# Kernel tuning notes

Hardware: AMD Instinct MI355X
Metric: run time of the kernel (lower is better)

The kernel has to match this reference:

```python
import jax, jax.numpy as jnp
import numpy as np
from jax import lax

B = 256; D_IN = 2048; HID = 2048; NSEG = 10; D_CTX = 1024; OUT = 100; NI = 205
KW_PCT = 0.05
K = int(round(KW_PCT * HID))  # 102 winners per sample per layer
W_DENSITY = 0.05      # weight_sparsity = 0.95
DEND_DENSITY = 0.05   # dendrite_weight_sparsity = 0.95


def setup_inputs() -> dict:
    key = jax.random.key(0)
    ks = jax.random.split(key, 16)
    def u(k, shape, bound):
        return jax.random.uniform(k, shape, minval=-bound, maxval=bound, dtype=jnp.float32)
    inp = {}
    inp["x"] = jax.random.normal(ks[0], (B, D_IN), jnp.float32)
    inp["context"] = jax.random.normal(ks[1], (B, D_CTX), jnp.float32)
    # layer 1 FF weights: modified kaiming, input density 1.0 -> bound = 1/sqrt(fan_in)
    inp["W1"] = u(ks[2], (HID, D_IN), 1.0 / np.sqrt(D_IN))
    inp["b1"] = jnp.zeros((HID,), jnp.float32)
    # dendrites: input density 1.0 (context_percent_on=1), weight density 0.05
    dend_bound = 1.0 / np.sqrt(DEND_DENSITY * D_CTX)
    inp["segW1"] = u(ks[3], (HID, NSEG, D_CTX), dend_bound)
    inp["maskW1"] = (jax.random.uniform(ks[4], (HID, D_IN)) < W_DENSITY).astype(jnp.float32)
    inp["maskS1"] = (jax.random.uniform(ks[5], (HID, NSEG, D_CTX)) < DEND_DENSITY).astype(jnp.float32)
    # layer 2 FF weights: input density = kw_percent_on (k-winners upstream)
    inp["W2"] = u(ks[6], (HID, HID), 1.0 / np.sqrt(KW_PCT * HID))
    inp["b2"] = jnp.zeros((HID,), jnp.float32)
    inp["segW2"] = u(ks[7], (HID, NSEG, D_CTX), dend_bound)
    inp["maskW2"] = (jax.random.uniform(ks[8], (HID, HID)) < W_DENSITY).astype(jnp.float32)
    inp["maskS2"] = (jax.random.uniform(ks[9], (HID, NSEG, D_CTX)) < DEND_DENSITY).astype(jnp.float32)
    # Dale (EiDense) output head: non-negative excitatory/inhibitory factors
    s = 1.0 / np.sqrt(HID)
    inp["Wex_out"] = jax.random.uniform(ks[10], (OUT, HID), dtype=jnp.float32) * s
    inp["Wix_out"] = jax.random.uniform(ks[11], (1, HID), dtype=jnp.float32) * s
    inp["Wei_out"] = jax.random.uniform(ks[12], (OUT, 1), dtype=jnp.float32)
    inp["b_out"] = jnp.zeros((OUT,), jnp.float32)
    return inp


def _kwinners(y, k):
    # keep top-k activations per row, zero the rest (boost_strength=0)
    vals, idxs = lax.top_k(y, k)  # [B, k]
    rows = jnp.arange(y.shape[0])[:, None]
    return jnp.zeros_like(y).at[rows, idxs].set(vals)


def _dendritic_layer(x, context, W, b, segW, maskW, maskS):
    # sparse-masked feedforward projection
    y = x @ (W * maskW).T + b  # [B, HID]
    # per-unit dendrite segment activations from context
    d = jnp.einsum('bc,usc->bus', context, segW * maskS)  # [B, HID, NSEG]
    # absolute-max gating: pick segment with max |activation|, gate by sigmoid
    sel = jnp.argmax(jnp.abs(d), axis=-1)  # [B, HID]
    chosen = jnp.take_along_axis(d, sel[..., None], axis=-1)[..., 0]
    y = y * jax.nn.sigmoid(chosen)
    return _kwinners(y, K)


def reference(x, context, W1, b1, segW1, maskW1, maskS1, W2, b2, segW2, maskW2, maskS2, Wex_out, Wix_out, Wei_out, b_out):
    h = _dendritic_layer(x, context, W1, b1, segW1, maskW1, maskS1)
    h = _dendritic_layer(h, context, W2, b2, segW2, maskW2, maskS2)
    # EiDense output head: W = Wex - Wei @ Wix (Dale's law), no output nonlinearity
    W_out = Wex_out - Wei_out @ Wix_out  # [OUT, HID]
    return h @ W_out.T + b_out
```

## Files before the change

### kernel.cpp

```cpp
#include <hip/hip_runtime.h>
#include <math.h>

#define B_SZ   256
#define D_IN   2048
#define HID    2048
#define NSEG   10
#define D_CTX  1024
#define OUT_N  100
#define KWIN   102
#define CAP    256

typedef float f32x4 __attribute__((ext_vector_type(4)));

__device__ __forceinline__ f32x4 ntld4(const float* p) {
  return __builtin_nontemporal_load((const f32x4*)p);
}

__device__ __forceinline__ unsigned f2key(float f) {
  unsigned b = __float_as_uint(f);
  return (b & 0x80000000u) ? ~b : (b | 0x80000000u);
}
__device__ __forceinline__ float key2f(unsigned k) {
  return (k & 0x80000000u) ? __uint_as_float(k & 0x7FFFFFFFu) : __uint_as_float(~k);
}

__global__ __launch_bounds__(256) void transpose2_k(const float* __restrict__ xsrc,
                                                    float* __restrict__ xdst,
                                                    const float* __restrict__ csrc,
                                                    float* __restrict__ cdst) {
  __shared__ float tile[32][33];
  int bid = blockIdx.x;
  const float* src; float* dst; int cols;
  const int NX = (D_IN / 32) * (B_SZ / 32);
  if (bid < NX) { src = xsrc; dst = xdst; cols = D_IN; }
  else { bid -= NX; src = csrc; dst = cdst; cols = D_CTX; }
  int nbx = cols / 32;
  int bx = bid % nbx, by = bid / nbx;
  int c0 = bx * 32, r0 = by * 32;
  int tx = threadIdx.x & 31, ty = threadIdx.x >> 5;
  for (int i = ty; i < 32; i += 8)
    tile[i][tx] = src[(r0 + i) * cols + (c0 + tx)];
  __syncthreads();
  for (int i = ty; i < 32; i += 8)
    dst[(c0 + i) * B_SZ + (r0 + tx)] = tile[tx][i];
}

__device__ __forceinline__ int compact_wave(const float* __restrict__ wrow,
                                            const float* __restrict__ mrow,
                                            int len4, float2* pairs, int* scnt) {
  const int t = threadIdx.x & 63;
  if (t == 0) *scnt = 0;
  __builtin_amdgcn_wave_barrier();
  for (int e = t; e < len4; e += 64) {
    f32x4 w = ntld4(wrow + 4 * e);
    f32x4 m = ntld4(mrow + 4 * e);
    bool n0 = (m.x != 0.f), n1 = (m.y != 0.f), n2 = (m.z != 0.f), n3 = (m.w != 0.f);
    int nz = (int)n0 + (int)n1 + (int)n2 + (int)n3;
    if (nz) {
      int pos = atomicAdd(scnt, nz);
      int c = e << 2;
      if (n0) { if (pos < CAP) pairs[pos] = make_float2(w.x, __int_as_float(c));     pos++; }
      if (n1) { if (pos < CAP) pairs[pos] = make_float2(w.y, __int_as_float(c + 1)); pos++; }
      if (n2) { if (pos < CAP) pairs[pos] = make_float2(w.z, __int_as_float(c + 2)); pos++; }
      if (n3) { if (pos < CAP) pairs[pos] = make_float2(w.w, __int_as_float(c + 3)); pos++; }
    }
  }
  __builtin_amdgcn_wave_barrier();
  int c = *scnt;
  return c > CAP ? CAP : c;
}

__device__ __forceinline__ int store_seg(const f32x4 w[4], const f32x4 m[4],
                                         float2* pairs, int* scnt) {
  const int t = threadIdx.x & 63;
  if (t == 0) *scnt = 0;
  __builtin_amdgcn_wave_barrier();
#pragma unroll
  for (int i = 0; i < 4; ++i) {
    int e = t + 64 * i;
    f32x4 ww = w[i], mm = m[i];
    bool n0 = (mm.x != 0.f), n1 = (mm.y != 0.f), n2 = (mm.z != 0.f), n3 = (mm.w != 0.f);
    int nz = (int)n0 + (int)n1 + (int)n2 + (int)n3;
    if (nz) {
      int pos = atomicAdd(scnt, nz);
      int c = e << 2;
      if (n0) { if (pos < CAP) pairs[pos] = make_float2(ww.x, __int_as_float(c));     pos++; }
      if (n1) { if (pos < CAP) pairs[pos] = make_float2(ww.y, __int_as_float(c + 1)); pos++; }
      if (n2) { if (pos < CAP) pairs[pos] = make_float2(ww.z, __int_as_float(c + 2)); pos++; }
      if (n3) { if (pos < CAP) pairs[pos] = make_float2(ww.w, __int_as_float(c + 3)); pos++; }
    }
  }
  __builtin_amdgcn_wave_barrier();
  int c = *scnt;
  return c > CAP ? CAP : c;
}

__device__ __forceinline__ void load_seg(const float* __restrict__ wrow,
                                         const float* __restrict__ mrow,
                                         f32x4 w[4], f32x4 m[4]) {
  const int t = threadIdx.x & 63;
#pragma unroll
  for (int i = 0; i < 4; ++i) {
    w[i] = ntld4(wrow + 4 * (t + 64 * i));
    m[i] = ntld4(mrow + 4 * (t + 64 * i));
  }
}

__device__ __forceinline__ void gather_dot(const float* __restrict__ src,
                                           const float2* pairs, int cnt,
                                           int t4, float out4[4]) {
  float acc[4][4];
#pragma unroll
  for (int s = 0; s < 4; ++s)
#pragma unroll
    for (int i = 0; i < 4; ++i) acc[s][i] = 0.f;
  int j = 0;
  for (; j + 8 <= cnt; j += 8) {
#pragma unroll
    for (int s = 0; s < 8; ++s) {
      float2 p = pairs[j + s];
      const f32x4 cv = *(const f32x4*)(src + (__float_as_int(p.y) << 8) + t4);
      acc[s & 3][0] += cv.x * p.x; acc[s & 3][1] += cv.y * p.x;
      acc[s & 3][2] += cv.z * p.x; acc[s & 3][3] += cv.w * p.x;
    }
  }
  for (; j < cnt; ++j) {
    float2 p = pairs[j];
    const f32x4 cv = *(const f32x4*)(src + (__float_as_int(p.y) << 8) + t4);
    acc[0][0] += cv.x * p.x; acc[0][1] += cv.y * p.x;
    acc[0][2] += cv.z * p.x; acc[0][3] += cv.w * p.x;
  }
#pragma unroll
  for (int i = 0; i < 4; ++i)
    out4[i] = (acc[0][i] + acc[1][i]) + (acc[2][i] + acc[3][i]);
}

__global__ __launch_bounds__(256, 3) void dend_kernel(
    const float* __restrict__ W1, const float* __restrict__ maskW1, const float* __restrict__ b1,
    const float* __restrict__ segW1, const float* __restrict__ maskS1,
    const float* __restrict__ segW2, const float* __restrict__ maskS2,
    const float* __restrict__ xT, const float* __restrict__ ctxT,
    float* __restrict__ y1T, float* __restrict__ gate2T) {
  __shared__ float2 pairs_s[4][CAP];
  __shared__ int scnt_s[4];
  const int wave = threadIdx.x >> 6;
  const int t = threadIdx.x & 63, t4 = t * 4;
  float2* pairs = pairs_s[wave];
  int* scnt = &scnt_s[wave];
  const int row = blockIdx.x * 4 + wave;

  const bool isL1 = (row < HID);
  const int u = isL1 ? row : (row - HID);
  const float* segW = (isL1 ? segW1 : segW2) + (size_t)u * NSEG * D_CTX;
  const float* maskS = (isL1 ? maskS1 : maskS2) + (size_t)u * NSEG * D_CTX;

  float bestA[4] = {-1.f, -1.f, -1.f, -1.f};
  float chosen[4] = {0.f, 0.f, 0.f, 0.f};
  float ff[4] = {0.f, 0.f, 0.f, 0.f};

  f32x4 w[4], m[4];
  if (isL1) {
    int cnt = compact_wave(W1 + (size_t)u * D_IN, maskW1 + (size_t)u * D_IN,
                           D_IN / 4, pairs, scnt);
    load_seg(segW, maskS, w, m);
    gather_dot(xT, pairs, cnt, t4, ff);
  } else {
    load_seg(segW, maskS, w, m);
  }

  for (int s = 0; s < NSEG; ++s) {
    int cnt = store_seg(w, m, pairs, scnt);
    if (s + 1 < NSEG)
      load_seg(segW + (s + 1) * D_CTX, maskS + (s + 1) * D_CTX, w, m);
    float d[4];
    gather_dot(ctxT, pairs, cnt, t4, d);
#pragma unroll
    for (int i = 0; i < 4; ++i) {
      float a = fabsf(d[i]);
      if (a > bestA[i]) { bestA[i] = a; chosen[i] = d[i]; }
    }
  }

  if (isL1) {
    float bb = b1[u];
    float4 o;
    o.x = (ff[0] + bb) / (1.f + expf(-chosen[0]));
    o.y = (ff[1] + bb) / (1.f + expf(-chosen[1]));
    o.z = (ff[2] + bb) / (1.f + expf(-chosen[2]));
    o.w = (ff[3] + bb) / (1.f + expf(-chosen[3]));
    *(float4*)(y1T + (size_t)u * B_SZ + t4) = o;
  } else {
    float4 g;
    g.x = 1.f / (1.f + expf(-chosen[0]));
    g.y = 1.f / (1.f + expf(-chosen[1]));
    g.z = 1.f / (1.f + expf(-chosen[2]));
    g.w = 1.f / (1.f + expf(-chosen[3]));
    *(float4*)(gate2T + (size_t)u * B_SZ + t4) = g;
  }
}

__global__ __launch_bounds__(256, 4) void ff2_kernel(
    const float* __restrict__ W2, const float* __restrict__ maskW2, const float* __restrict__ b2,
    const float* __restrict__ h1T, const float* __restrict__ gate2T, float* __restrict__ y2T) {
  __shared__ float2 pairs_s[4][CAP];
  __shared__ int scnt_s[4];
  const int wave = threadIdx.x >> 6;
  const int t = threadIdx.x & 63, t4 = t * 4;
  const int u = blockIdx.x * 4 + wave;
  int cnt = compact_wave(W2 + (size_t)u * HID, maskW2 + (size_t)u * HID,
                         HID / 4, pairs_s[wave], &scnt_s[wave]);
  float acc[4];
  gather_dot(h1T, pairs_s[wave], cnt, t4, acc);
  float bb = b2[u];
  float4 g = *(const float4*)(gate2T + (size_t)u * B_SZ + t4);
  float4 o;
  o.x = (acc[0] + bb) * g.x; o.y = (acc[1] + bb) * g.y;
  o.z = (acc[2] + bb) * g.z; o.w = (acc[3] + bb) * g.w;
  *(float4*)(y2T + (size_t)u * B_SZ + t4) = o;
}

__global__ __launch_bounds__(256) void topk_kernel(const float* __restrict__ yT,
                                                   float* __restrict__ dst, int mode) {
  const int b = blockIdx.x, t = threadIdx.x;
  __shared__ int hist[256];
  __shared__ int sfx[256];
  __shared__ unsigned sPref;
  __shared__ int sRem;
  unsigned myk[8];
#pragma unroll
  for (int i = 0; i < 8; ++i)
    myk[i] = f2key(yT[(size_t)(t * 8 + i) * B_SZ + b]);
  unsigned pref = 0;
  int rem = KWIN;
  for (int shift = 24; shift >= 0; shift -= 8) {
    hist[t] = 0;
    __syncthreads();
    unsigned hiMask = (shift == 24) ? 0u : (0xFFFFFFFFu << (shift + 8));
#pragma unroll
    for (int i = 0; i < 8; ++i) {
      unsigned k = myk[i];
      if ((k & hiMask) == pref) atomicAdd(&hist[(k >> shift) & 255], 1);
    }
    __syncthreads();
    sfx[t] = hist[t];
    __syncthreads();
    for (int off = 1; off < 256; off <<= 1) {
      int add = (t + off < 256) ? sfx[t + off] : 0;
      __syncthreads();
      sfx[t] += add;
      __syncthreads();
    }
    int s_incl = sfx[t];
    int s_excl = (t == 255) ? 0 : sfx[t + 1];
    if (s_incl >= rem && s_excl < rem) {
      sPref = pref | (((unsigned)t) << shift);
      sRem = rem - s_excl;
    }
    __syncthreads();
    pref = sPref;
    rem = sRem;
    __syncthreads();
  }
  int eq = 0;
#pragma unroll
  for (int i = 0; i < 8; ++i) eq += (myk[i] == pref) ? 1 : 0;
  sfx[t] = eq;
  __syncthreads();
  for (int off = 1; off < 256; off <<= 1) {
    int add = (t >= off) ? sfx[t - off] : 0;
    __syncthreads();
    sfx[t] += add;
    __syncthreads();
  }
  int excl = sfx[t] - eq;
  int taken = 0;
#pragma unroll
  for (int i = 0; i < 8; ++i) {
    unsigned k = myk[i];
    bool keep;
    if (k > pref) keep = true;
    else if (k == pref) { keep = (excl + taken) < rem; taken++; }
    else keep = false;
    float f = keep ? key2f(k) : 0.f;
    int uu = t * 8 + i;
    if (mode == 0) dst[(size_t)uu * B_SZ + b] = f;
    else dst[(size_t)b * HID + uu] = f;
  }
}

__global__ __launch_bounds__(256) void out_kernel(
    const float* __restrict__ h2, const float* __restrict__ Wex, const float* __restrict__ Wix,
    const float* __restrict__ Wei, const float* __restrict__ bo, float* __restrict__ out) {
  const int b = blockIdx.x, t = threadIdx.x;
  __shared__ float hrow[HID];
  __shared__ float red[256];
  float part = 0.f;
#pragma unroll
  for (int i = 0; i < 8; ++i) {
    int u = t + 256 * i;
    float v = h2[(size_t)b * HID + u];
    hrow[u] = v;
    part += v * Wix[u];
  }
  red[t] = part;
  __syncthreads();
  for (int off = 128; off > 0; off >>= 1) {
    if (t < off) red[t] += red[t + off];
    __syncthreads();
  }
  float S = red[0];
  const int w = t >> 6, l = t & 63;
  for (int o = w; o < OUT_N; o += 4) {
    float acc = 0.f;
    const float* wr = Wex + (size_t)o * HID;
#pragma unroll
    for (int q = 0; q < HID / 64; ++q) acc += hrow[l + 64 * q] * wr[l + 64 * q];
    for (int off = 32; off > 0; off >>= 1) acc += __shfl_down(acc, off, 64);
    if (l == 0) out[(size_t)b * OUT_N + o] = acc - Wei[o] * S + bo[o];
  }
}

extern "C" void kernel_launch(void* const* d_in, const int* in_sizes, int n_in,
                              void* d_out, int out_size, void* d_ws, size_t ws_size,
                              hipStream_t stream) {
  const float* x      = (const float*)d_in[0];
  const float* ctx    = (const float*)d_in[1];
  const float* W1     = (const float*)d_in[2];
  const float* b1     = (const float*)d_in[3];
  const float* segW1  = (const float*)d_in[4];
  const float* maskW1 = (const float*)d_in[5];
  const float* maskS1 = (const float*)d_in[6];
  const float* W2     = (const float*)d_in[7];
  const float* b2     = (const float*)d_in[8];
  const float* segW2  = (const float*)d_in[9];
  const float* maskW2 = (const float*)d_in[10];
  const float* maskS2 = (const float*)d_in[11];
  const float* Wex    = (const float*)d_in[12];
  const float* Wix    = (const float*)d_in[13];
  const float* Wei    = (const float*)d_in[14];
  const float* bo     = (const float*)d_in[15];
  float* out = (float*)d_out;
  float* ws = (float*)d_ws;

  float* xT     = ws;
  float* ctxT   = ws + 524288;
  float* y1T    = ws + 786432;
  float* gate2T = ws + 1310720;
  float* y2T    = ws + 1835008;
  float* h2     = ws + 2359296;

  transpose2_k<<<768, 256, 0, stream>>>(x, xT, ctx, ctxT);
  dend_kernel<<<2 * HID / 4, 256, 0, stream>>>(W1, maskW1, b1, segW1, maskS1, segW2, maskS2,
                                               xT, ctxT, y1T, gate2T);
  topk_kernel<<<B_SZ, 256, 0, stream>>>(y1T, y1T, 0);
  ff2_kernel<<<HID / 4, 256, 0, stream>>>(W2, maskW2, b2, y1T, gate2T, y2T);
  topk_kernel<<<B_SZ, 256, 0, stream>>>(y2T, h2, 1);
  out_kernel<<<B_SZ, 256, 0, stream>>>(h2, Wex, Wix, Wei, bo, out);
}
```

Measured before the change: 498.0 us.

## Split dendrite segments across two waves, ballot-based compaction, separate FF1 kernel

Dendrite gate computation now assigns each unit to two waves that each handle five segments and merge their argmax results through shared memory, which doubles the number of waves working in parallel. Atomic-based sparse compaction is replaced with wave ballot plus popcount prefix sums. The layer-1 feedforward moves out of the dendrite kernel into a generic ff_kernel that is reused for both layers, and gate1 shares a workspace slot with y2. The trade-off is one extra launch and an extra round trip of the gate array through memory, and the per-segment pair capacity is cut to 128.

```diff
diff --git a/kernel.cpp b/kernel.cpp
--- a/kernel.cpp
+++ b/kernel.cpp
@@ -9,6 +9,7 @@
 #define OUT_N  100
 #define KWIN   102
 #define CAP    256
+#define CAPS   128
 
 typedef float f32x4 __attribute__((ext_vector_type(4)));
 
@@ -45,67 +46,6 @@
     dst[(c0 + i) * B_SZ + (r0 + tx)] = tile[tx][i];
 }
 
-__device__ __forceinline__ int compact_wave(const float* __restrict__ wrow,
-                                            const float* __restrict__ mrow,
-                                            int len4, float2* pairs, int* scnt) {
-  const int t = threadIdx.x & 63;
-  if (t == 0) *scnt = 0;
-  __builtin_amdgcn_wave_barrier();
-  for (int e = t; e < len4; e += 64) {
-    f32x4 w = ntld4(wrow + 4 * e);
-    f32x4 m = ntld4(mrow + 4 * e);
-    bool n0 = (m.x != 0.f), n1 = (m.y != 0.f), n2 = (m.z != 0.f), n3 = (m.w != 0.f);
-    int nz = (int)n0 + (int)n1 + (int)n2 + (int)n3;
-    if (nz) {
-      int pos = atomicAdd(scnt, nz);
-      int c = e << 2;
-      if (n0) { if (pos < CAP) pairs[pos] = make_float2(w.x, __int_as_float(c));     pos++; }
-      if (n1) { if (pos < CAP) pairs[pos] = make_float2(w.y, __int_as_float(c + 1)); pos++; }
-      if (n2) { if (pos < CAP) pairs[pos] = make_float2(w.z, __int_as_float(c + 2)); pos++; }
-      if (n3) { if (pos < CAP) pairs[pos] = make_float2(w.w, __int_as_float(c + 3)); pos++; }
-    }
-  }
-  __builtin_amdgcn_wave_barrier();
-  int c = *scnt;
-  return c > CAP ? CAP : c;
-}
-
-__device__ __forceinline__ int store_seg(const f32x4 w[4], const f32x4 m[4],
-                                         float2* pairs, int* scnt) {
-  const int t = threadIdx.x & 63;
-  if (t == 0) *scnt = 0;
-  __builtin_amdgcn_wave_barrier();
-#pragma unroll
-  for (int i = 0; i < 4; ++i) {
-    int e = t + 64 * i;
-    f32x4 ww = w[i], mm = m[i];
-    bool n0 = (mm.x != 0.f), n1 = (mm.y != 0.f), n2 = (mm.z != 0.f), n3 = (mm.w != 0.f);
-    int nz = (int)n0 + (int)n1 + (int)n2 + (int)n3;
-    if (nz) {
-      int pos = atomicAdd(scnt, nz);
-      int c = e << 2;
-      if (n0) { if (pos < CAP) pairs[pos] = make_float2(ww.x, __int_as_float(c));     pos++; }
-      if (n1) { if (pos < CAP) pairs[pos] = make_float2(ww.y, __int_as_float(c + 1)); pos++; }
-      if (n2) { if (pos < CAP) pairs[pos] = make_float2(ww.z, __int_as_float(c + 2)); pos++; }
-      if (n3) { if (pos < CAP) pairs[pos] = make_float2(ww.w, __int_as_float(c + 3)); pos++; }
-    }
-  }
-  __builtin_amdgcn_wave_barrier();
-  int c = *scnt;
-  return c > CAP ? CAP : c;
-}
-
-__device__ __forceinline__ void load_seg(const float* __restrict__ wrow,
-                                         const float* __restrict__ mrow,
-                                         f32x4 w[4], f32x4 m[4]) {
-  const int t = threadIdx.x & 63;
-#pragma unroll
-  for (int i = 0; i < 4; ++i) {
-    w[i] = ntld4(wrow + 4 * (t + 64 * i));
-    m[i] = ntld4(mrow + 4 * (t + 64 * i));
-  }
-}
-
 __device__ __forceinline__ void gather_dot(const float* __restrict__ src,
                                            const float2* pairs, int cnt,
                                            int t4, float out4[4]) {
@@ -135,42 +75,71 @@
     out4[i] = (acc[0][i] + acc[1][i]) + (acc[2][i] + acc[3][i]);
 }
 
-__global__ __launch_bounds__(256, 3) void dend_kernel(
-    const float* __restrict__ W1, const float* __restrict__ maskW1, const float* __restrict__ b1,
+__device__ __forceinline__ void load_seg(const float* __restrict__ wrow,
+                                         const float* __restrict__ mrow,
+                                         f32x4 w[4], f32x4 m[4]) {
+  const int t = threadIdx.x & 63;
+#pragma unroll
+  for (int i = 0; i < 4; ++i) {
+    w[i] = ntld4(wrow + 4 * (t + 64 * i));
+    m[i] = ntld4(mrow + 4 * (t + 64 * i));
+  }
+}
+
+__device__ __forceinline__ int store_seg_ballot(const f32x4 w[4], const f32x4 m[4],
+                                                float2* pairs) {
+  const int t = threadIdx.x & 63;
+  const unsigned long long below = (1ull << t) - 1ull;
+  int base = 0;
+#pragma unroll
+  for (int i = 0; i < 4; ++i) {
+    const int c = (t + 64 * i) << 2;
+    const float wv[4] = {w[i].x, w[i].y, w[i].z, w[i].w};
+    const float mv[4] = {m[i].x, m[i].y, m[i].z, m[i].w};
+#pragma unroll
+    for (int j = 0; j < 4; ++j) {
+      bool nz = (mv[j] != 0.f);
+      unsigned long long bal = __ballot(nz);
+      if (nz) {
+        int pos = base + (int)__popcll(bal & below);
+        if (pos < CAPS) pairs[pos] = make_float2(wv[j], __int_as_float(c + j));
+      }
+      base += (int)__popcll(bal);
+    }
+  }
+  __builtin_amdgcn_wave_barrier();
+  return base > CAPS ? CAPS : base;
+}
+
+__global__ __launch_bounds__(256, 4) void dend_gates_kernel(
     const float* __restrict__ segW1, const float* __restrict__ maskS1,
     const float* __restrict__ segW2, const float* __restrict__ maskS2,
-    const float* __restrict__ xT, const float* __restrict__ ctxT,
-    float* __restrict__ y1T, float* __restrict__ gate2T) {
-  __shared__ float2 pairs_s[4][CAP];
-  __shared__ int scnt_s[4];
+    const float* __restrict__ ctxT,
+    float* __restrict__ gate1T, float* __restrict__ gate2T) {
+  __shared__ float2 pairs_s[4][CAPS];
+  __shared__ float exch[2][64][9];
   const int wave = threadIdx.x >> 6;
   const int t = threadIdx.x & 63, t4 = t * 4;
-  float2* pairs = pairs_s[wave];
-  int* scnt = &scnt_s[wave];
-  const int row = blockIdx.x * 4 + wave;
-
+  const int pidx = wave >> 1;
+  const int half = wave & 1;
+  const int row = blockIdx.x * 2 + pidx;
   const bool isL1 = (row < HID);
   const int u = isL1 ? row : (row - HID);
-  const float* segW = (isL1 ? segW1 : segW2) + (size_t)u * NSEG * D_CTX;
-  const float* maskS = (isL1 ? maskS1 : maskS2) + (size_t)u * NSEG * D_CTX;
+  const float* segW = (isL1 ? segW1 : segW2)
+                      + (size_t)u * NSEG * D_CTX + (size_t)half * 5 * D_CTX;
+  const float* maskS = (isL1 ? maskS1 : maskS2)
+                      + (size_t)u * NSEG * D_CTX + (size_t)half * 5 * D_CTX;
+  float2* pairs = pairs_s[wave];
 
   float bestA[4] = {-1.f, -1.f, -1.f, -1.f};
   float chosen[4] = {0.f, 0.f, 0.f, 0.f};
-  float ff[4] = {0.f, 0.f, 0.f, 0.f};
 
   f32x4 w[4], m[4];
-  if (isL1) {
-    int cnt = compact_wave(W1 + (size_t)u * D_IN, maskW1 + (size_t)u * D_IN,
-                           D_IN / 4, pairs, scnt);
-    load_seg(segW, maskS, w, m);
-    gather_dot(xT, pairs, cnt, t4, ff);
-  } else {
-    load_seg(segW, maskS, w, m);
-  }
-
-  for (int s = 0; s < NSEG; ++s) {
-    int cnt = store_seg(w, m, pairs, scnt);
-    if (s + 1 < NSEG)
+  load_seg(segW, maskS, w, m);
+#pragma unroll 1
+  for (int s = 0; s < 5; ++s) {
+    int cnt = store_seg_ballot(w, m, pairs);
+    if (s + 1 < 5)
       load_seg(segW + (s + 1) * D_CTX, maskS + (s + 1) * D_CTX, w, m);
     float d[4];
     gather_dot(ctxT, pairs, cnt, t4, d);
@@ -181,42 +150,69 @@
     }
   }
 
-  if (isL1) {
-    float bb = b1[u];
-    float4 o;
-    o.x = (ff[0] + bb) / (1.f + expf(-chosen[0]));
-    o.y = (ff[1] + bb) / (1.f + expf(-chosen[1]));
-    o.z = (ff[2] + bb) / (1.f + expf(-chosen[2]));
-    o.w = (ff[3] + bb) / (1.f + expf(-chosen[3]));
-    *(float4*)(y1T + (size_t)u * B_SZ + t4) = o;
-  } else {
+  if (half) {
+#pragma unroll
+    for (int i = 0; i < 4; ++i) {
+      exch[pidx][t][i] = bestA[i];
+      exch[pidx][t][4 + i] = chosen[i];
+    }
+  }
+  __syncthreads();
+  if (!half) {
+#pragma unroll
+    for (int i = 0; i < 4; ++i) {
+      float a1 = exch[pidx][t][i];
+      if (a1 > bestA[i]) chosen[i] = exch[pidx][t][4 + i];
+    }
     float4 g;
     g.x = 1.f / (1.f + expf(-chosen[0]));
     g.y = 1.f / (1.f + expf(-chosen[1]));
     g.z = 1.f / (1.f + expf(-chosen[2]));
     g.w = 1.f / (1.f + expf(-chosen[3]));
-    *(float4*)(gate2T + (size_t)u * B_SZ + t4) = g;
-  }
-}
-
-__global__ __launch_bounds__(256, 4) void ff2_kernel(
-    const float* __restrict__ W2, const float* __restrict__ maskW2, const float* __restrict__ b2,
-    const float* __restrict__ h1T, const float* __restrict__ gate2T, float* __restrict__ y2T) {
+    float* gT = isL1 ? gate1T : gate2T;
+    *(float4*)(gT + (size_t)u * B_SZ + t4) = g;
+  }
+}
+
+__global__ __launch_bounds__(256, 4) void ff_kernel(
+    const float* __restrict__ W, const float* __restrict__ maskW, const float* __restrict__ b,
+    const float* __restrict__ srcT, const float* __restrict__ gateT, float* __restrict__ yT) {
   __shared__ float2 pairs_s[4][CAP];
-  __shared__ int scnt_s[4];
   const int wave = threadIdx.x >> 6;
   const int t = threadIdx.x & 63, t4 = t * 4;
   const int u = blockIdx.x * 4 + wave;
-  int cnt = compact_wave(W2 + (size_t)u * HID, maskW2 + (size_t)u * HID,
-                         HID / 4, pairs_s[wave], &scnt_s[wave]);
+  float2* pairs = pairs_s[wave];
+  const float* wrow = W + (size_t)u * HID;
+  const float* mrow = maskW + (size_t)u * HID;
+  const unsigned long long below = (1ull << t) - 1ull;
+  int base = 0;
+  for (int e = t; e < HID / 4; e += 64) {
+    f32x4 ww = ntld4(wrow + 4 * e);
+    f32x4 mm = ntld4(mrow + 4 * e);
+    const float wv[4] = {ww.x, ww.y, ww.z, ww.w};
+    const float mv[4] = {mm.x, mm.y, mm.z, mm.w};
+    const int c = e << 2;
+#pragma unroll
+    for (int j = 0; j < 4; ++j) {
+      bool nz = (mv[j] != 0.f);
+      unsigned long long bal = __ballot(nz);
+      if (nz) {
+        int pos = base + (int)__popcll(bal & below);
+        if (pos < CAP) pairs[pos] = make_float2(wv[j], __int_as_float(c + j));
+      }
+      base += (int)__popcll(bal);
+    }
+  }
+  __builtin_amdgcn_wave_barrier();
+  int cnt = base > CAP ? CAP : base;
   float acc[4];
-  gather_dot(h1T, pairs_s[wave], cnt, t4, acc);
-  float bb = b2[u];
-  float4 g = *(const float4*)(gate2T + (size_t)u * B_SZ + t4);
+  gather_dot(srcT, pairs, cnt, t4, acc);
+  float bb = b[u];
+  float4 g = *(const float4*)(gateT + (size_t)u * B_SZ + t4);
   float4 o;
   o.x = (acc[0] + bb) * g.x; o.y = (acc[1] + bb) * g.y;
   o.z = (acc[2] + bb) * g.z; o.w = (acc[3] + bb) * g.w;
-  *(float4*)(y2T + (size_t)u * B_SZ + t4) = o;
+  *(float4*)(yT + (size_t)u * B_SZ + t4) = o;
 }
 
 __global__ __launch_bounds__(256) void topk_kernel(const float* __restrict__ yT,
@@ -346,14 +342,17 @@
   float* ctxT   = ws + 524288;
   float* y1T    = ws + 786432;
   float* gate2T = ws + 1310720;
-  float* y2T    = ws + 1835008;
+  float* slotA  = ws + 1835008;
   float* h2     = ws + 2359296;
+  float* gate1T = slotA;
+  float* y2T    = slotA;
 
   transpose2_k<<<768, 256, 0, stream>>>(x, xT, ctx, ctxT);
-  dend_kernel<<<2 * HID / 4, 256, 0, stream>>>(W1, maskW1, b1, segW1, maskS1, segW2, maskS2,
-                                               xT, ctxT, y1T, gate2T);
+  dend_gates_kernel<<<2 * HID / 2, 256, 0, stream>>>(segW1, maskS1, segW2, maskS2,
+                                                     ctxT, gate1T, gate2T);
+  ff_kernel<<<HID / 4, 256, 0, stream>>>(W1, maskW1, b1, xT, gate1T, y1T);
   topk_kernel<<<B_SZ, 256, 0, stream>>>(y1T, y1T, 0);
-  ff2_kernel<<<HID / 4, 256, 0, stream>>>(W2, maskW2, b2, y1T, gate2T, y2T);
+  ff_kernel<<<HID / 4, 256, 0, stream>>>(W2, maskW2, b2, y1T, gate2T, y2T);
   topk_kernel<<<B_SZ, 256, 0, stream>>>(y2T, h2, 1);
   out_kernel<<<B_SZ, 256, 0, stream>>>(h2, Wex, Wix, Wei, bo, out);
 }
```

Result: slower. 524.4 us (+5.3%).
